# Optimization experiments

Hardware: AMD Instinct MI355X
Metric: run time of the kernel (lower is better)

The kernel has to match this reference:

```python
import jax, jax.numpy as jnp
import numpy as np

N_NODES = 100000
N_EDGES = 3200000
IN_DIM, HID_DIM, OUT_DIM = 128, 128, 64
NUM_LAYERS = 5


def setup_inputs() -> dict:
    key = jax.random.key(0)
    ks = jax.random.split(key, 2 + 2 * NUM_LAYERS)
    h = jax.random.normal(ks[0], (N_NODES, IN_DIM), dtype=jnp.float32)
    edge_index = jax.random.randint(ks[1], (2, N_EDGES), 0, N_NODES, dtype=jnp.int64)
    dims = [IN_DIM] + [HID_DIM] * (NUM_LAYERS - 1) + [OUT_DIM]
    inp = {"h": h, "edge_index": edge_index}
    for i in range(NUM_LAYERS):
        fan_in = dims[i]
        bound = 1.0 / np.sqrt(fan_in)
        inp[f"W{i}"] = jax.random.uniform(ks[2 + 2 * i], (dims[i], dims[i + 1]), jnp.float32, -bound, bound)
        inp[f"b{i}"] = jax.random.uniform(ks[3 + 2 * i], (dims[i + 1],), jnp.float32, -bound, bound)
    return inp


def _gin_layer(h, src, dst, W, b):
    # sum aggregation: agg[v] = sum_{(u->v) in E} h[u]
    agg = jax.ops.segment_sum(h[src], dst, num_segments=N_NODES)
    # eps = 0, learn_eps = False: rst = (1 + 0) * h + agg, then MLP (single Linear)
    return (h + agg) @ W + b


def reference(h, edge_index, W0, b0, W1, b1, W2, b2, W3, b3, W4, b4):
    src, dst = edge_index[0], edge_index[1]
    Ws = [W0, W1, W2, W3, W4]
    bs = [b0, b1, b2, b3, b4]
    for i in range(NUM_LAYERS):
        h = _gin_layer(h, src, dst, Ws[i], bs[i])
    return h
```

## Files before the change

kernel.cpp:

```cpp
#include <hip/hip_runtime.h>

#define N_NODES 100000
#define N_EDGES 3200000
#define NB 782
#define BCAP 5120
#define CHUNK_EDGES 4096
#define NCHUNKS ((N_EDGES + CHUNK_EDGES - 1) / CHUNK_EDGES)

typedef unsigned int uint;
typedef __attribute__((ext_vector_type(4))) uint u4v;
typedef __attribute__((ext_vector_type(2))) float f2v;
typedef __attribute__((ext_vector_type(8))) short s8v;
typedef __attribute__((ext_vector_type(4))) float f32x4;


__global__ void detect_fmt(const uint* __restrict__ e, int* __restrict__ flag,
                           int* __restrict__ row_ptr) {
    if (threadIdx.x == 0) {
        *flag = (e[1] == 0u && e[3] == 0u && e[5] == 0u && e[7] == 0u) ? 1 : 0;
        row_ptr[N_NODES] = N_EDGES;
    }
}

__device__ __forceinline__ int load_idx(const void* edges, int fmt, long long i) {
    return fmt ? (int)((const long long*)edges)[i] : ((const int*)edges)[i];
}

__global__ __launch_bounds__(256) void part_hist(const void* __restrict__ edges,
                                                 const int* __restrict__ flag,
                                                 int* __restrict__ hist2,
                                                 int* __restrict__ bcount) {
    __shared__ int cnt[NB];
    for (int i = threadIdx.x; i < NB; i += 256) cnt[i] = 0;
    __syncthreads();
    int fmt = *flag;
    int c = blockIdx.x;
    int beg = c * CHUNK_EDGES, end = min(beg + CHUNK_EDGES, N_EDGES);
    for (int i = beg + threadIdx.x; i < end; i += 256) {
        int dst = load_idx(edges, fmt, (long long)N_EDGES + i);
        atomicAdd(&cnt[dst >> 7], 1);
    }
    __syncthreads();
    for (int i = threadIdx.x; i < NB; i += 256) {
        hist2[c * NB + i] = cnt[i];
        if (cnt[i]) atomicAdd(&bcount[i], cnt[i]);
    }
}

__global__ void scan_kernel(const int* __restrict__ count, int* __restrict__ off_out, int n) {
    __shared__ int sums[1024];
    int t = threadIdx.x;
    int chunk = (n + 1023) >> 10;
    int beg = t * chunk;
    int end = min(beg + chunk, n);
    int s = 0;
    for (int i = beg; i < end; ++i) s += count[i];
    sums[t] = s;
    __syncthreads();
    int val = s;
    for (int off = 1; off < 1024; off <<= 1) {
        int other = (t >= off) ? sums[t - off] : 0;
        __syncthreads();
        val += other;
        sums[t] = val;
        __syncthreads();
    }
    int run = val - s;
    for (int i = beg; i < end; ++i) {
        off_out[i] = run;
        run += count[i];
    }
    if (end >= n) off_out[n] = run;
}

__global__ __launch_bounds__(1024) void chunk_scan(const int* __restrict__ hist2,
                                                   const int* __restrict__ boff,
                                                   int* __restrict__ base2) {
    __shared__ int s[1024];
    int b = blockIdx.x;
    int t = threadIdx.x;
    int v = (t < NCHUNKS) ? hist2[t * NB + b] : 0;
    s[t] = v;
    __syncthreads();
    int val = v;
    for (int off = 1; off < 1024; off <<= 1) {
        int o = (t >= off) ? s[t - off] : 0;
        __syncthreads();
        val += o;
        s[t] = val;
        __syncthreads();
    }
    if (t < NCHUNKS) base2[t * NB + b] = boff[b] + val - v;
}

__global__ __launch_bounds__(256) void part_scatter(const void* __restrict__ edges,
                                                    const int* __restrict__ flag,
                                                    const int* __restrict__ base2,
                                                    uint* __restrict__ tmp) {
    __shared__ int cur[NB];
    int c = blockIdx.x;
    for (int i = threadIdx.x; i < NB; i += 256) cur[i] = base2[c * NB + i];
    __syncthreads();
    int fmt = *flag;
    int beg = c * CHUNK_EDGES, end = min(beg + CHUNK_EDGES, N_EDGES);
    for (int i = beg + threadIdx.x; i < end; i += 256) {
        int src = load_idx(edges, fmt, i);
        int dst = load_idx(edges, fmt, (long long)N_EDGES + i);
        int b = dst >> 7;
        int pos = atomicAdd(&cur[b], 1);
        tmp[pos] = ((uint)(dst & 127) << 17) | (uint)src;
    }
}

__global__ __launch_bounds__(256) void bucket_finalize(const uint* __restrict__ tmp,
                                                       const int* __restrict__ boff,
                                                       int* __restrict__ row_ptr,
                                                       int* __restrict__ esorted) {
    __shared__ uint s1[BCAP];
    __shared__ int s2[BCAP];
    __shared__ int cnt[128], pref[128], cur[128];
    int b = blockIdx.x;
    int beg = boff[b];
    int n = boff[b + 1] - beg;
    if (n > BCAP) n = BCAP;
    int t = threadIdx.x;
    if (t < 128) cnt[t] = 0;
    __syncthreads();
    for (int e = t; e < n; e += 256) {
        uint k = tmp[beg + e];
        s1[e] = k;
        atomicAdd(&cnt[k >> 17], 1);
    }
    __syncthreads();
    if (t < 128) pref[t] = cnt[t];
    __syncthreads();
    for (int off = 1; off < 128; off <<= 1) {
        int v = (t < 128 && t >= off) ? pref[t - off] : 0;
        __syncthreads();
        if (t < 128) pref[t] += v;
        __syncthreads();
    }
    if (t < 128) {
        int ex = pref[t] - cnt[t];
        cur[t] = ex;
        int node = b * 128 + t;
        if (node < N_NODES) row_ptr[node] = beg + ex;
    }
    __syncthreads();
    for (int e = t; e < n; e += 256) {
        uint k = s1[e];
        int p = atomicAdd(&cur[k >> 17], 1);
        s2[p] = (int)(k & 0x1FFFF);
    }
    __syncthreads();
    for (int e = t; e < n; e += 256) esorted[beg + e] = s2[e];
}


__device__ __forceinline__ uint bf16pack(float a, float b) {
    uint ua = __float_as_uint(a);
    ua = (ua + 0x7FFFu + ((ua >> 16) & 1u)) >> 16;
    uint ub = __float_as_uint(b);
    ub = (ub + 0x7FFFu + ((ub >> 16) & 1u)) >> 16;
    return ua | (ub << 16);
}
__device__ __forceinline__ float bf_lo(uint u) { return __uint_as_float(u << 16); }
__device__ __forceinline__ float bf_hi(uint u) { return __uint_as_float(u & 0xFFFF0000u); }


__global__ __launch_bounds__(256) void matstage(const float* __restrict__ Wl,
                                                const float* __restrict__ bl,
                                                const float* __restrict__ Sin,
                                                float* __restrict__ Sout,
                                                float* __restrict__ cout) {
    __shared__ float S[128 * 64];
    int tid = threadIdx.x;
    int b = blockIdx.x;
    for (int i = tid; i < 128 * 16; i += 256) ((float4*)S)[i] = ((const float4*)Sin)[i];
    __syncthreads();
    if (b < 32) {
        int rr = tid >> 6;
        int c = tid & 63;
        int r = b * 4 + rr;
        const float* wrow = &Wl[r * 128];
        float s = 0.f;
#pragma unroll 8
        for (int k = 0; k < 128; ++k) s += wrow[k] * S[k * 64 + c];
        Sout[r * 64 + c] = s;
    } else if (tid < 64) {
        float s = 0.f;
        for (int k = 0; k < 128; ++k) s += bl[k] * S[k * 64 + tid];
        cout[tid] = s;
    }
}

__global__ __launch_bounds__(256) void prep_z(const float* __restrict__ S0,
                                              const float* __restrict__ b4,
                                              u4v* __restrict__ Wt,
                                              float* __restrict__ c_all) {
    int idx = blockIdx.x * 256 + threadIdx.x;
    if (blockIdx.x == 0 && threadIdx.x < 64) c_all[4 * 64 + threadIdx.x] = b4[threadIdx.x];
    if (idx >= 64 * 16) return;
    int n = idx >> 4, c16 = idx & 15;
    u4v o;
#pragma unroll
    for (int q = 0; q < 4; ++q)
        o[q] = bf16pack(S0[(size_t)(c16 * 8 + 2 * q) * 64 + n],
                        S0[(size_t)(c16 * 8 + 2 * q + 1) * 64 + n]);
    Wt[n * 16 + (c16 ^ (n & 7))] = o;
}


__global__ __launch_bounds__(256) void agg64_step(const uint* __restrict__ z,
                                                  const int* __restrict__ row_ptr,
                                                  const int* __restrict__ esrc,
                                                  const float* __restrict__ cvec,
                                                  uint* __restrict__ zn) {
    int lane = threadIdx.x & 63;
    int l32 = lane & 31;
    int half = lane >> 5;
    int wid = (blockIdx.x * blockDim.x + threadIdx.x) >> 6;
    int nw = (gridDim.x * blockDim.x) >> 6;
    f2v cc = ((const f2v*)cvec)[l32];
    for (int v = wid; v < N_NODES; v += nw) {
        f2v a = {0.f, 0.f};
        int beg = row_ptr[v], end = row_ptr[v + 1];
        int i = beg;
        for (; i + 16 <= end; i += 16) {
            uint k[8], u[8];
#pragma unroll
            for (int j = 0; j < 8; ++j) k[j] = (uint)esrc[i + 2 * j + half];
#pragma unroll
            for (int j = 0; j < 8; ++j) u[j] = z[k[j] * 32u + (uint)l32];
#pragma unroll
            for (int j = 0; j < 8; ++j) {
                f2v t = {bf_lo(u[j]), bf_hi(u[j])};
                a += t;
            }
        }
        for (; i < end; i += 2) {
            int idx = i + half;
            uint uu = 0u;
            if (idx < end) uu = z[(uint)esrc[idx] * 32u + (uint)l32];
            f2v t = {bf_lo(uu), bf_hi(uu)};
            a += t;
        }
        a.x += __shfl_xor(a.x, 32);
        a.y += __shfl_xor(a.y, 32);
        if (half == 0) {
            uint self = z[(uint)v * 32u + (uint)l32];
            __builtin_nontemporal_store(
                bf16pack(a.x + bf_lo(self) + cc.x, a.y + bf_hi(self) + cc.y),
                &zn[(uint)v * 32u + (uint)l32]);
        }
    }
}

__global__ __launch_bounds__(256) void agg64_last(const uint* __restrict__ z,
                                                  const int* __restrict__ row_ptr,
                                                  const int* __restrict__ esrc,
                                                  const float* __restrict__ cvec,
                                                  float* __restrict__ out) {
    int lane = threadIdx.x & 63;
    int l32 = lane & 31;
    int half = lane >> 5;
    int wid = (blockIdx.x * blockDim.x + threadIdx.x) >> 6;
    int nw = (gridDim.x * blockDim.x) >> 6;
    f2v cc = ((const f2v*)cvec)[l32];
    for (int v = wid; v < N_NODES; v += nw) {
        f2v a = {0.f, 0.f};
        int beg = row_ptr[v], end = row_ptr[v + 1];
        int i = beg;
        for (; i + 16 <= end; i += 16) {
            uint k[8], u[8];
#pragma unroll
            for (int j = 0; j < 8; ++j) k[j] = (uint)esrc[i + 2 * j + half];
#pragma unroll
            for (int j = 0; j < 8; ++j) u[j] = z[k[j] * 32u + (uint)l32];
#pragma unroll
            for (int j = 0; j < 8; ++j) {
                f2v t = {bf_lo(u[j]), bf_hi(u[j])};
                a += t;
            }
        }
        for (; i < end; i += 2) {
            int idx = i + half;
            uint uu = 0u;
            if (idx < end) uu = z[(uint)esrc[idx] * 32u + (uint)l32];
            f2v t = {bf_lo(uu), bf_hi(uu)};
            a += t;
        }
        a.x += __shfl_xor(a.x, 32);
        a.y += __shfl_xor(a.y, 32);
        if (half == 0) {
            uint self = z[(uint)v * 32u + (uint)l32];
            f2v o = {a.x + bf_lo(self) + cc.x, a.y + bf_hi(self) + cc.y};
            __builtin_nontemporal_store(o, &((f2v*)out)[(uint)v * 32u + (uint)l32]);
        }
    }
}


__global__ __launch_bounds__(256) void mfma_gemm64(const float* __restrict__ x,
                                                   const u4v* __restrict__ Wt,
                                                   uint* __restrict__ y) {
    constexpr int SMEM = 32768 + 64 * 256;
    __shared__ char raw[SMEM];
    u4v* Asm = (u4v*)raw;
    u4v* Bsm = (u4v*)(raw + 32768);
    float* Cst = (float*)raw;
    int tid = threadIdx.x;
    int m0 = blockIdx.x * 128;

#pragma unroll
    for (int i = 0; i < 8; ++i) {
        int idx = tid + i * 256;
        int r = idx >> 4, c16 = idx & 15;
        int m = m0 + r;
        if (m >= N_NODES) m = N_NODES - 1;
        const float* src = &x[(size_t)m * 128 + c16 * 8];
        float4 v0 = *(const float4*)src;
        float4 v1 = *(const float4*)(src + 4);
        u4v o = {bf16pack(v0.x, v0.y), bf16pack(v0.z, v0.w),
                 bf16pack(v1.x, v1.y), bf16pack(v1.z, v1.w)};
        Asm[r * 16 + (c16 ^ (r & 7))] = o;
    }
#pragma unroll
    for (int i = 0; i < 4; ++i) Bsm[tid + i * 256] = Wt[tid + i * 256];
    __syncthreads();

    int lane = tid & 63;
    int w = tid >> 6;
    int n0w = w * 16;
    int lhi = lane >> 4, llo = lane & 15;
    f32x4 acc[8];
#pragma unroll
    for (int i = 0; i < 8; ++i) acc[i] = (f32x4){0.f, 0.f, 0.f, 0.f};

#pragma unroll
    for (int ks = 0; ks < 4; ++ks) {
        int cb = ks * 4 + lhi;
        int col = n0w + llo;
        u4v tb = Bsm[col * 16 + (cb ^ (col & 7))];
        s8v bfr = *(s8v*)&tb;
#pragma unroll
        for (int i = 0; i < 8; ++i) {
            int row = i * 16 + llo;
            u4v t = Asm[row * 16 + (cb ^ (row & 7))];
            s8v aa = *(s8v*)&t;
            acc[i] = __builtin_amdgcn_mfma_f32_16x16x32_bf16(aa, bfr, acc[i], 0, 0, 0);
        }
    }
    __syncthreads();
#pragma unroll
    for (int i = 0; i < 8; ++i)
#pragma unroll
        for (int r = 0; r < 4; ++r)
            Cst[(i * 16 + lhi * 4 + r) * 64 + n0w + llo] = acc[i][r];
    __syncthreads();
#pragma unroll
    for (int i = 0; i < 16; ++i) {
        int idx = tid + i * 256;
        int m = idx >> 5, np = idx & 31;
        if (m0 + m < N_NODES)
            y[(size_t)(m0 + m) * 32 + np] =
                bf16pack(Cst[m * 64 + 2 * np], Cst[m * 64 + 2 * np + 1]);
    }
}

extern "C" void kernel_launch(void* const* d_in, const int* in_sizes, int n_in,
                              void* d_out, int out_size, void* d_ws, size_t ws_size,
                              hipStream_t stream) {
    const float* h_in = (const float*)d_in[0];
    const void* edges = d_in[1];
    const float* W[5] = {(const float*)d_in[2], (const float*)d_in[4], (const float*)d_in[6],
                         (const float*)d_in[8], (const float*)d_in[10]};
    const float* B[5] = {(const float*)d_in[3], (const float*)d_in[5], (const float*)d_in[7],
                         (const float*)d_in[9], (const float*)d_in[11]};

    size_t off = 0;
    auto alloc = [&](size_t bytes) {
        void* p = (char*)d_ws + off;
        off = (off + bytes + 255) & ~(size_t)255;
        return p;
    };
    int* esorted = (int*)alloc((size_t)N_EDGES * 4);
    int* row_ptr = (int*)alloc((size_t)(N_NODES + 1) * 4);
    int* hist2 = (int*)alloc((size_t)NCHUNKS * NB * 4);
    int* base2 = (int*)alloc((size_t)NCHUNKS * NB * 4);
    int* bcount = (int*)alloc((size_t)NB * 4);
    int* boff = (int*)alloc((size_t)(NB + 1) * 4);
    int* flag = (int*)alloc(256);
    float* Sa = (float*)alloc(128 * 64 * 4);
    float* Sb = (float*)alloc(128 * 64 * 4);
    float* c_all = (float*)alloc(5 * 64 * 4);
    u4v* Wt_z = (u4v*)alloc((size_t)64 * 16 * 16);
    uint* zA = (uint*)alloc((size_t)N_NODES * 32 * 4);
    uint* zB = (uint*)alloc((size_t)N_NODES * 32 * 4);
    uint* tmp = (uint*)alloc((size_t)N_EDGES * 4);

    detect_fmt<<<1, 64, 0, stream>>>((const uint*)edges, flag, row_ptr);
    hipMemsetAsync(bcount, 0, (size_t)NB * 4, stream);
    part_hist<<<NCHUNKS, 256, 0, stream>>>(edges, flag, hist2, bcount);
    scan_kernel<<<1, 1024, 0, stream>>>(bcount, boff, NB);
    chunk_scan<<<NB, 1024, 0, stream>>>(hist2, boff, base2);
    part_scatter<<<NCHUNKS, 256, 0, stream>>>(edges, flag, base2, tmp);
    bucket_finalize<<<NB, 256, 0, stream>>>(tmp, boff, row_ptr, esorted);

    matstage<<<33, 256, 0, stream>>>(W[3], B[3], W[4], Sa, c_all + 3 * 64);
    matstage<<<33, 256, 0, stream>>>(W[2], B[2], Sa, Sb, c_all + 2 * 64);
    matstage<<<33, 256, 0, stream>>>(W[1], B[1], Sb, Sa, c_all + 1 * 64);
    matstage<<<33, 256, 0, stream>>>(W[0], B[0], Sa, Sb, c_all + 0 * 64);
    prep_z<<<4, 256, 0, stream>>>(Sb, B[4], Wt_z, c_all);

    mfma_gemm64<<<(N_NODES + 127) / 128, 256, 0, stream>>>(h_in, Wt_z, zA);
    agg64_step<<<2048, 256, 0, stream>>>(zA, row_ptr, esorted, c_all + 0 * 64, zB);
    agg64_step<<<2048, 256, 0, stream>>>(zB, row_ptr, esorted, c_all + 1 * 64, zA);
    agg64_step<<<2048, 256, 0, stream>>>(zA, row_ptr, esorted, c_all + 2 * 64, zB);
    agg64_step<<<2048, 256, 0, stream>>>(zB, row_ptr, esorted, c_all + 3 * 64, zA);
    agg64_last<<<2048, 256, 0, stream>>>(zA, row_ptr, esorted, c_all + 4 * 64,
                                         (float*)d_out);
}
```

Before: 504.6 us.

## Widen aggregation gathers to 8-byte loads and transpose chunk histogram layout

The aggregation kernels now give each lane two packed bf16 pairs (8 bytes) and have four 16-lane groups work on different edges at once, instead of two 32-lane halves doing 4-byte loads. This gives more edges in flight per wave with wider memory transactions, and needs an extra shuffle reduction stage. The per-chunk histogram is also stored bucket-major, so chunk_scan reads contiguous memory instead of strided. Other edits are cosmetic type swaps.

```diff
diff --git a/kernel.cpp b/kernel.cpp
--- a/kernel.cpp
+++ b/kernel.cpp
@@ -8,8 +8,10 @@
 #define NCHUNKS ((N_EDGES + CHUNK_EDGES - 1) / CHUNK_EDGES)
 
 typedef unsigned int uint;
+typedef __attribute__((ext_vector_type(2))) uint u2v;
 typedef __attribute__((ext_vector_type(4))) uint u4v;
 typedef __attribute__((ext_vector_type(2))) float f2v;
+typedef __attribute__((ext_vector_type(4))) float f4v;
 typedef __attribute__((ext_vector_type(8))) short s8v;
 typedef __attribute__((ext_vector_type(4))) float f32x4;
 
@@ -42,7 +44,7 @@
     }
     __syncthreads();
     for (int i = threadIdx.x; i < NB; i += 256) {
-        hist2[c * NB + i] = cnt[i];
+        hist2[i * NCHUNKS + c] = cnt[i];
         if (cnt[i]) atomicAdd(&bcount[i], cnt[i]);
     }
 }
@@ -79,7 +81,7 @@
     __shared__ int s[1024];
     int b = blockIdx.x;
     int t = threadIdx.x;
-    int v = (t < NCHUNKS) ? hist2[t * NB + b] : 0;
+    int v = (t < NCHUNKS) ? hist2[b * NCHUNKS + t] : 0;
     s[t] = v;
     __syncthreads();
     int val = v;
@@ -176,7 +178,7 @@
     __shared__ float S[128 * 64];
     int tid = threadIdx.x;
     int b = blockIdx.x;
-    for (int i = tid; i < 128 * 16; i += 256) ((float4*)S)[i] = ((const float4*)Sin)[i];
+    for (int i = tid; i < 128 * 16; i += 256) ((f4v*)S)[i] = ((const f4v*)Sin)[i];
     __syncthreads();
     if (b < 32) {
         int rr = tid >> 6;
@@ -216,42 +218,54 @@
                                                   const int* __restrict__ esrc,
                                                   const float* __restrict__ cvec,
                                                   uint* __restrict__ zn) {
+    const u2v* z2 = (const u2v*)z;
     int lane = threadIdx.x & 63;
-    int l32 = lane & 31;
-    int half = lane >> 5;
+    int c = lane & 15;
+    int g = lane >> 4;
     int wid = (blockIdx.x * blockDim.x + threadIdx.x) >> 6;
     int nw = (gridDim.x * blockDim.x) >> 6;
-    f2v cc = ((const f2v*)cvec)[l32];
+    f4v cc = ((const f4v*)cvec)[c];
     for (int v = wid; v < N_NODES; v += nw) {
-        f2v a = {0.f, 0.f};
+        f2v aX = {0.f, 0.f}, aY = {0.f, 0.f};
         int beg = row_ptr[v], end = row_ptr[v + 1];
         int i = beg;
         for (; i + 16 <= end; i += 16) {
-            uint k[8], u[8];
-#pragma unroll
-            for (int j = 0; j < 8; ++j) k[j] = (uint)esrc[i + 2 * j + half];
-#pragma unroll
-            for (int j = 0; j < 8; ++j) u[j] = z[k[j] * 32u + (uint)l32];
-#pragma unroll
-            for (int j = 0; j < 8; ++j) {
-                f2v t = {bf_lo(u[j]), bf_hi(u[j])};
-                a += t;
+            uint k[4];
+            u2v u[4];
+#pragma unroll
+            for (int j = 0; j < 4; ++j) k[j] = (uint)esrc[i + 4 * j + g];
+#pragma unroll
+            for (int j = 0; j < 4; ++j) u[j] = z2[k[j] * 16u + (uint)c];
+#pragma unroll
+            for (int j = 0; j < 4; ++j) {
+                f2v t0 = {bf_lo(u[j].x), bf_hi(u[j].x)};
+                f2v t1 = {bf_lo(u[j].y), bf_hi(u[j].y)};
+                aX += t0;
+                aY += t1;
             }
         }
-        for (; i < end; i += 2) {
-            int idx = i + half;
-            uint uu = 0u;
-            if (idx < end) uu = z[(uint)esrc[idx] * 32u + (uint)l32];
-            f2v t = {bf_lo(uu), bf_hi(uu)};
-            a += t;
-        }
-        a.x += __shfl_xor(a.x, 32);
-        a.y += __shfl_xor(a.y, 32);
-        if (half == 0) {
-            uint self = z[(uint)v * 32u + (uint)l32];
-            __builtin_nontemporal_store(
-                bf16pack(a.x + bf_lo(self) + cc.x, a.y + bf_hi(self) + cc.y),
-                &zn[(uint)v * 32u + (uint)l32]);
+        for (; i < end; i += 4) {
+            int idx = i + g;
+            u2v uu = {0u, 0u};
+            if (idx < end) uu = z2[(uint)esrc[idx] * 16u + (uint)c];
+            f2v t0 = {bf_lo(uu.x), bf_hi(uu.x)};
+            f2v t1 = {bf_lo(uu.y), bf_hi(uu.y)};
+            aX += t0;
+            aY += t1;
+        }
+        aX.x += __shfl_xor(aX.x, 16);
+        aX.y += __shfl_xor(aX.y, 16);
+        aY.x += __shfl_xor(aY.x, 16);
+        aY.y += __shfl_xor(aY.y, 16);
+        aX.x += __shfl_xor(aX.x, 32);
+        aX.y += __shfl_xor(aX.y, 32);
+        aY.x += __shfl_xor(aY.x, 32);
+        aY.y += __shfl_xor(aY.y, 32);
+        if (g == 0) {
+            u2v self = z2[(uint)v * 16u + (uint)c];
+            u2v o = {bf16pack(aX.x + bf_lo(self.x) + cc.x, aX.y + bf_hi(self.x) + cc.y),
+                     bf16pack(aY.x + bf_lo(self.y) + cc.z, aY.y + bf_hi(self.y) + cc.w)};
+            __builtin_nontemporal_store(o, &((u2v*)zn)[(uint)v * 16u + (uint)c]);
         }
     }
 }
@@ -261,41 +275,54 @@
                                                   const int* __restrict__ esrc,
                                                   const float* __restrict__ cvec,
                                                   float* __restrict__ out) {
+    const u2v* z2 = (const u2v*)z;
     int lane = threadIdx.x & 63;
-    int l32 = lane & 31;
-    int half = lane >> 5;
+    int c = lane & 15;
+    int g = lane >> 4;
     int wid = (blockIdx.x * blockDim.x + threadIdx.x) >> 6;
     int nw = (gridDim.x * blockDim.x) >> 6;
-    f2v cc = ((const f2v*)cvec)[l32];
+    f4v cc = ((const f4v*)cvec)[c];
     for (int v = wid; v < N_NODES; v += nw) {
-        f2v a = {0.f, 0.f};
+        f2v aX = {0.f, 0.f}, aY = {0.f, 0.f};
         int beg = row_ptr[v], end = row_ptr[v + 1];
         int i = beg;
         for (; i + 16 <= end; i += 16) {
-            uint k[8], u[8];
-#pragma unroll
-            for (int j = 0; j < 8; ++j) k[j] = (uint)esrc[i + 2 * j + half];
-#pragma unroll
-            for (int j = 0; j < 8; ++j) u[j] = z[k[j] * 32u + (uint)l32];
-#pragma unroll
-            for (int j = 0; j < 8; ++j) {
-                f2v t = {bf_lo(u[j]), bf_hi(u[j])};
-                a += t;
+            uint k[4];
+            u2v u[4];
+#pragma unroll
+            for (int j = 0; j < 4; ++j) k[j] = (uint)esrc[i + 4 * j + g];
+#pragma unroll
+            for (int j = 0; j < 4; ++j) u[j] = z2[k[j] * 16u + (uint)c];
+#pragma unroll
+            for (int j = 0; j < 4; ++j) {
+                f2v t0 = {bf_lo(u[j].x), bf_hi(u[j].x)};
+                f2v t1 = {bf_lo(u[j].y), bf_hi(u[j].y)};
+                aX += t0;
+                aY += t1;
             }
         }
-        for (; i < end; i += 2) {
-            int idx = i + half;
-            uint uu = 0u;
-            if (idx < end) uu = z[(uint)esrc[idx] * 32u + (uint)l32];
-            f2v t = {bf_lo(uu), bf_hi(uu)};
-            a += t;
-        }
-        a.x += __shfl_xor(a.x, 32);
-        a.y += __shfl_xor(a.y, 32);
-        if (half == 0) {
-            uint self = z[(uint)v * 32u + (uint)l32];
-            f2v o = {a.x + bf_lo(self) + cc.x, a.y + bf_hi(self) + cc.y};
-            __builtin_nontemporal_store(o, &((f2v*)out)[(uint)v * 32u + (uint)l32]);
+        for (; i < end; i += 4) {
+            int idx = i + g;
+            u2v uu = {0u, 0u};
+            if (idx < end) uu = z2[(uint)esrc[idx] * 16u + (uint)c];
+            f2v t0 = {bf_lo(uu.x), bf_hi(uu.x)};
+            f2v t1 = {bf_lo(uu.y), bf_hi(uu.y)};
+            aX += t0;
+            aY += t1;
+        }
+        aX.x += __shfl_xor(aX.x, 16);
+        aX.y += __shfl_xor(aX.y, 16);
+        aY.x += __shfl_xor(aY.x, 16);
+        aY.y += __shfl_xor(aY.y, 16);
+        aX.x += __shfl_xor(aX.x, 32);
+        aX.y += __shfl_xor(aX.y, 32);
+        aY.x += __shfl_xor(aY.x, 32);
+        aY.y += __shfl_xor(aY.y, 32);
+        if (g == 0) {
+            u2v self = z2[(uint)v * 16u + (uint)c];
+            f4v o = {aX.x + bf_lo(self.x) + cc.x, aX.y + bf_hi(self.x) + cc.y,
+                     aY.x + bf_lo(self.y) + cc.z, aY.y + bf_hi(self.y) + cc.w};
+            __builtin_nontemporal_store(o, &((f4v*)out)[(uint)v * 16u + (uint)c]);
         }
     }
 }
@@ -319,8 +346,8 @@
         int m = m0 + r;
         if (m >= N_NODES) m = N_NODES - 1;
         const float* src = &x[(size_t)m * 128 + c16 * 8];
-        float4 v0 = *(const float4*)src;
-        float4 v1 = *(const float4*)(src + 4);
+        f4v v0 = *(const f4v*)src;
+        f4v v1 = *(const f4v*)(src + 4);
         u4v o = {bf16pack(v0.x, v0.y), bf16pack(v0.z, v0.w),
                  bf16pack(v1.x, v1.y), bf16pack(v1.z, v1.w)};
         Asm[r * 16 + (c16 ^ (r & 7))] = o;
@@ -400,7 +427,7 @@
     uint* tmp = (uint*)alloc((size_t)N_EDGES * 4);
 
     detect_fmt<<<1, 64, 0, stream>>>((const uint*)edges, flag, row_ptr);
-    hipMemsetAsync(bcount, 0, (size_t)NB * 4, stream);
+    (void)hipMemsetAsync(bcount, 0, (size_t)NB * 4, stream);
     part_hist<<<NCHUNKS, 256, 0, stream>>>(edges, flag, hist2, bcount);
     scan_kernel<<<1, 1024, 0, stream>>>(bcount, boff, NB);
     chunk_scan<<<NB, 1024, 0, stream>>>(hist2, boff, base2);
```

Measured after the change: 438.2 us. 13.2% less time.
